# Performance work log

Hardware: AMD Instinct MI355X
Metric: run time of the kernel (lower is better)

Reference implementation:

```python
import jax, jax.numpy as jnp
import numpy as np

B = 256   # batch == nodes (required by the module's mask broadcasting)
N = 256
F = 128   # in_features
H = 4     # num_heads
D = 8     # out_features (per-head dim)
E_RAND = 8192


def setup_inputs() -> dict:
    key = jax.random.key(0)
    ks = jax.random.split(key, 10)
    x = jax.random.normal(ks[0], (B, N, F), jnp.float32)
    # random edges + self-loops so every adjacency row is non-empty
    e = jax.random.randint(ks[1], (2, E_RAND), 0, B)
    diag = jnp.stack([jnp.arange(B), jnp.arange(B)])
    edge_index = jnp.concatenate([e, diag], axis=1)  # [2, 8448]
    s_in = 1.0 / np.sqrt(F)
    s_hd = 1.0 / np.sqrt(H * D)
    Wq = jax.random.normal(ks[2], (F, H * D), jnp.float32) * s_in
    Wk = jax.random.normal(ks[3], (F, H * D), jnp.float32) * s_in
    Wv = jax.random.normal(ks[4], (F, H * D), jnp.float32) * s_in
    Wo = jax.random.normal(ks[5], (H * D, D), jnp.float32) * s_hd
    bq = jax.random.normal(ks[6], (H * D,), jnp.float32) * s_in
    bk = jax.random.normal(ks[7], (H * D,), jnp.float32) * s_in
    bv = jax.random.normal(ks[8], (H * D,), jnp.float32) * s_in
    bo = jax.random.normal(ks[9], (D,), jnp.float32) * s_hd
    return dict(x=x, edge_index=edge_index, Wq=Wq, bq=bq, Wk=Wk, bk=bk,
                Wv=Wv, bv=bv, Wo=Wo, bo=bo)


def reference(x, edge_index, Wq, bq, Wk, bk, Wv, bv, Wo, bo):
    Bn, Nn, _ = x.shape
    q = (x @ Wq + bq).reshape(Bn, Nn, H, D)
    k = (x @ Wk + bk).reshape(Bn, Nn, H, D)
    v = (x @ Wv + bv).reshape(Bn, Nn, H, D)
    # [B, H, N, N]
    scores = jnp.einsum('bqhd,bkhd->bhqk', q, k) / jnp.sqrt(jnp.float32(D))
    # dense adjacency from sparse edge list, as in the original
    adj = jnp.zeros((Bn, Bn), x.dtype).at[edge_index[0], edge_index[1]].set(1.0)
    # mask [B,B] broadcasts over trailing (q,k) dims since N == B
    scores = jnp.where(adj == 0, -jnp.inf, scores)
    attn = jax.nn.softmax(scores, axis=-1)
    out = jnp.einsum('bhqk,bkhd->bqhd', attn, v).reshape(Bn, Nn, H * D)
    return out @ Wo + bo
```

## Files before the change

### kernel.cpp

```cpp
#include <hip/hip_runtime.h>

typedef unsigned int u32;
typedef __fp16 h2v __attribute__((ext_vector_type(2)));
typedef __fp16 h4 __attribute__((ext_vector_type(4)));
typedef float f32x16 __attribute__((ext_vector_type(16)));

#define NB 256
#define NNODE 256
#define FF 128
#define DD 8
#define HDIM 32

__device__ __forceinline__ float dot2(h2v a, h2v b, float c) {
  return __builtin_amdgcn_fdot2(a, b, c, false);
}
__device__ __forceinline__ h2v bch2(u32 u) { return __builtin_bit_cast(h2v, u); }
__device__ __forceinline__ h4 bch4(uint2 u) { return __builtin_bit_cast(h4, u); }
__device__ __forceinline__ u32 bcu(h2v v) { return __builtin_bit_cast(u32, v); }
__device__ __forceinline__ f32x16 fzero() {
  f32x16 z;
  #pragma unroll
  for (int r = 0; r < 16; ++r) z[r] = 0.f;
  return z;
}
__device__ __forceinline__ f32x16 mfma8(h4 a, h4 b, f32x16 c) {
  return __builtin_amdgcn_mfma_f32_32x32x8f16(a, b, c, 0, 0, 0);
}

__global__ __launch_bounds__(256) void prep_kernel(
    const float* __restrict__ Wq, const float* __restrict__ bq,
    const float* __restrict__ Wk, const float* __restrict__ bk,
    const float* __restrict__ Wv, const float* __restrict__ bv,
    const float* __restrict__ Wo, const int* __restrict__ eidx, int E,
    u32* __restrict__ mask, u32* __restrict__ WtH, float* __restrict__ bias,
    u32* __restrict__ woT2)
{
  int g = blockIdx.x * 256 + threadIdx.x;
  if (g < 96 * 64) {
    int c = g >> 6, f = (g & 63) * 2;
    const float* W = (c < 32) ? Wq : ((c < 64) ? Wk : Wv);
    int cc = c & 31;
    WtH[g] = bcu(__builtin_amdgcn_cvt_pkrtz(W[f*HDIM + cc], W[(f+1)*HDIM + cc]));
  }
  if (g < 96) {
    const float* bb = (g < 32) ? bq : ((g < 64) ? bk : bv);
    bias[g] = bb[g & 31];
  }
  if (g < 128) {
    int d = g >> 4, p = g & 15;
    woT2[g] = bcu(__builtin_amdgcn_cvt_pkrtz(Wo[(2*p)*DD + d], Wo[(2*p+1)*DD + d]));
  }
  if (g < E) {
    int r = eidx[g], c = eidx[E + g];
    atomicOr(&mask[r*8 + (c >> 5)], 1u << (c & 31));
  }
}

__global__ __launch_bounds__(256, 2) void fused_kernel(
    const float* __restrict__ x, const u32* __restrict__ WtH,
    const float* __restrict__ bias, const u32* __restrict__ mask,
    const u32* __restrict__ woT2, const float* __restrict__ bo,
    float* __restrict__ out)
{
  __shared__ u32 wLds[96 * 66];
  __shared__ __fp16 kS[NNODE * 36];
  __shared__ __fp16 vt32[32 * 260];
  __shared__ __fp16 oS[128 * 36];
  __shared__ u32 woS[128];
  __shared__ float boS[8];

  int t = threadIdx.x, lane = t & 63, w = t >> 6;
  int l31 = lane & 31, hi = lane >> 5;
  int b = blockIdx.x & 255, half = blockIdx.x >> 8;

  for (int g = t; g < 96 * 64; g += 256)
    wLds[(g >> 6) * 66 + (g & 63)] = WtH[g];
  if (t < 128) woS[t] = woT2[t];
  if (t < 8) boS[t] = bo[t];

  f32x16 aq, ak0, av0, ak1, av1;
  #pragma unroll
  for (int r = 0; r < 16; ++r) aq[r] = bias[(r & 3) + 8*(r >> 2) + 4*hi];
  {
    float bk_ = bias[32 + l31], bv_ = bias[64 + l31];
    #pragma unroll
    for (int r = 0; r < 16; ++r) { ak0[r]=bk_; av0[r]=bv_; ak1[r]=bk_; av1[r]=bv_; }
  }

  int node = half*128 + w*32 + l31;
  uint4 m0 = *(const uint4*)(mask + node * 8);
  uint4 m1 = *(const uint4*)(mask + node * 8 + 4);
  u32 mw8[8] = { m0.x, m0.y, m0.z, m0.w, m1.x, m1.y, m1.z, m1.w };
  #pragma unroll
  for (int i = 0; i < 8; ++i) mw8[i] = hi ? (mw8[i] >> 4) : mw8[i];

  __syncthreads();

  const float* xr0 = x + ((size_t)b * NNODE + w*32 + l31) * FF + 4 * hi;
  const float* xr1 = xr0 + (size_t)128 * FF;
  float4 xc0 = *(const float4*)(xr0);
  float4 xc1 = *(const float4*)(xr1);
  #pragma unroll
  for (int ks = 0; ks < 16; ++ks) {
    float4 xn0, xn1;
    if (ks < 15) {
      xn0 = *(const float4*)(xr0 + (ks + 1) * 8);
      xn1 = *(const float4*)(xr1 + (ks + 1) * 8);
    }
    h2v a0 = __builtin_amdgcn_cvt_pkrtz(xc0.x, xc0.y);
    h2v b0 = __builtin_amdgcn_cvt_pkrtz(xc0.z, xc0.w);
    h4 f0 = __builtin_shufflevector(a0, b0, 0, 1, 2, 3);
    h2v a1 = __builtin_amdgcn_cvt_pkrtz(xc1.x, xc1.y);
    h2v b1 = __builtin_amdgcn_cvt_pkrtz(xc1.z, xc1.w);
    h4 f1 = __builtin_shufflevector(a1, b1, 0, 1, 2, 3);
    h4 wk = bch4(*(const uint2*)&wLds[(32 + l31)*66 + ks*4 + 2*hi]);
    h4 wv = bch4(*(const uint2*)&wLds[(64 + l31)*66 + ks*4 + 2*hi]);
    h4 wq = bch4(*(const uint2*)&wLds[l31*66 + ks*4 + 2*hi]);
    ak0 = mfma8(f0, wk, ak0);
    ak1 = mfma8(f1, wk, ak1);
    av0 = mfma8(f0, wv, av0);
    av1 = mfma8(f1, wv, av1);
    aq  = mfma8(wq, half ? f1 : f0, aq);
    xc0 = xn0; xc1 = xn1;
  }
  #pragma unroll
  for (int r = 0; r < 16; ++r) {
    int rc = (r & 3) + 8*(r >> 2) + 4*hi;
    int n0 = w*32 + rc, n1 = n0 + 128;
    kS[n0 * 36 + l31] = (__fp16)ak0[r];
    kS[n1 * 36 + l31] = (__fp16)ak1[r];
    vt32[l31 * 260 + n0] = (__fp16)av0[r];
    vt32[l31 * 260 + n1] = (__fp16)av1[r];
  }
  h4 Qf[4];
  #pragma unroll
  for (int h = 0; h < 4; ++h) {
    h2v qa = __builtin_amdgcn_cvt_pkrtz(aq[4*h],     aq[4*h + 1]);
    h2v qb = __builtin_amdgcn_cvt_pkrtz(aq[4*h + 2], aq[4*h + 3]);
    Qf[h] = __builtin_shufflevector(qa, qb, 0, 1, 2, 3);
  }
  __syncthreads();

  const float sc2 = 0.51006977f;
  const h2v one2 = bch2(0x3C003C00u);
  f32x16 accO[4] = { fzero(), fzero(), fzero(), fzero() };
  float lp[4] = { 0.f, 0.f, 0.f, 0.f };
  #pragma unroll
  for (int kt = 0; kt < 8; ++kt) {
    u32 mwh = mw8[kt];
    float mbv[16];
    #pragma unroll
    for (int r = 0; r < 16; ++r) {
      int bp = (r & 3) + 8*(r >> 2);
      mbv[r] = ((mwh >> bp) & 1u) ? -8.0f : -1e30f;
    }
    u32 pw[4][8];
    #pragma unroll
    for (int h = 0; h < 4; ++h) {
      h4 Kf = bch4(*(const uint2*)&kS[(kt*32 + l31)*36 + 8*h + 4*hi]);
      f32x16 T = mfma8(Kf, Qf[h], fzero());
      #pragma unroll
      for (int j = 0; j < 8; ++j) {
        float p0 = __builtin_amdgcn_exp2f(__builtin_fmaf(T[2*j],   sc2, mbv[2*j]));
        float p1 = __builtin_amdgcn_exp2f(__builtin_fmaf(T[2*j+1], sc2, mbv[2*j+1]));
        pw[h][j] = bcu(__builtin_amdgcn_cvt_pkrtz(p0, p1));
        lp[h] = dot2(bch2(pw[h][j]), one2, lp[h]);
      }
    }
    __builtin_amdgcn_s_setprio(1);
    #pragma unroll
    for (int kk = 0; kk < 4; ++kk) {
      h4 va = bch4(*(const uint2*)&vt32[l31*260 + kt*32 + kk*8 + 4*hi]);
      #pragma unroll
      for (int h = 0; h < 4; ++h)
        accO[h] = mfma8(va, bch4(make_uint2(pw[h][2*kk], pw[h][2*kk+1])), accO[h]);
    }
    __builtin_amdgcn_s_setprio(0);
  }
  #pragma unroll
  for (int h = 0; h < 4; ++h) {
    float lq = lp[h] + __shfl_xor(lp[h], 32);
    float inv = 1.0f / lq;
    h2v o0 = __builtin_amdgcn_cvt_pkrtz(accO[h][4*h]*inv,   accO[h][4*h+1]*inv);
    h2v o1 = __builtin_amdgcn_cvt_pkrtz(accO[h][4*h+2]*inv, accO[h][4*h+3]*inv);
    *(uint2*)&oS[(w*32 + l31)*36 + 8*h + 4*hi] = make_uint2(bcu(o0), bcu(o1));
  }
  __syncthreads();

  int pr = t >> 1, d4 = (t & 1) * 4;
  float r4[4] = { boS[d4], boS[d4+1], boS[d4+2], boS[d4+3] };
  #pragma unroll
  for (int p = 0; p < 16; ++p) {
    h2v o2 = bch2(*(const u32*)&oS[pr*36 + 2*p]);
    #pragma unroll
    for (int d = 0; d < 4; ++d)
      r4[d] = dot2(o2, bch2(woS[(d4 + d)*16 + p]), r4[d]);
  }
  float4 o = { r4[0], r4[1], r4[2], r4[3] };
  *(float4*)(out + ((size_t)b * NNODE + half*128 + pr) * DD + d4) = o;
}

extern "C" void kernel_launch(void* const* d_in, const int* in_sizes, int n_in,
                              void* d_out, int out_size, void* d_ws, size_t ws_size,
                              hipStream_t stream)
{
  const float* x  = (const float*)d_in[0];
  const int*   ei = (const int*)d_in[1];
  const float* Wq = (const float*)d_in[2];
  const float* bq = (const float*)d_in[3];
  const float* Wk = (const float*)d_in[4];
  const float* bk = (const float*)d_in[5];
  const float* Wv = (const float*)d_in[6];
  const float* bv = (const float*)d_in[7];
  const float* Wo = (const float*)d_in[8];
  const float* bo = (const float*)d_in[9];
  int E = in_sizes[1] / 2;

  char* ws = (char*)d_ws;
  u32*   mask = (u32*)(ws + 0);
  u32*   WtH  = (u32*)(ws + 8192);
  float* bias = (float*)(ws + 32768);
  u32*   woT2 = (u32*)(ws + 33280);

  hipMemsetAsync(mask, 0, NNODE * 8 * sizeof(u32), stream);
  int prep_work = (96*64 > E) ? 96*64 : E;
  prep_kernel<<<(prep_work + 255)/256, 256, 0, stream>>>(
      Wq, bq, Wk, bk, Wv, bv, Wo, ei, E, mask, WtH, bias, woT2);
  fused_kernel<<<NB * 2, 256, 0, stream>>>(x, WtH, bias, mask, woT2, bo,
                                           (float*)d_out);
}
```

Before: 39.50 us.

## Switch to 32x32x16 f16 MFMA with permlane32 swaps for P operand

Replaces the 32x32x8 f16 MFMA with the gfx950 32x32x16 variant in both the QKV projection and the PV product, halving the instruction count. The P fragments produced by the score MFMA are rearranged across lane halves with v_permlane32_swap so they match the wider K operand layout. LDS pads change to fit 16-byte reads, and the output staging buffer now reuses the weight LDS region to cut shared memory. This risks layout mistakes in the swap mapping and adds permute instructions to the inner loop.

```diff
diff --git a/kernel.cpp b/kernel.cpp
--- a/kernel.cpp
+++ b/kernel.cpp
@@ -3,6 +3,7 @@
 typedef unsigned int u32;
 typedef __fp16 h2v __attribute__((ext_vector_type(2)));
 typedef __fp16 h4 __attribute__((ext_vector_type(4)));
+typedef __fp16 h8 __attribute__((ext_vector_type(8)));
 typedef float f32x16 __attribute__((ext_vector_type(16)));
 
 #define NB 256
@@ -16,6 +17,7 @@
 }
 __device__ __forceinline__ h2v bch2(u32 u) { return __builtin_bit_cast(h2v, u); }
 __device__ __forceinline__ h4 bch4(uint2 u) { return __builtin_bit_cast(h4, u); }
+__device__ __forceinline__ h8 bch8(uint4 u) { return __builtin_bit_cast(h8, u); }
 __device__ __forceinline__ u32 bcu(h2v v) { return __builtin_bit_cast(u32, v); }
 __device__ __forceinline__ f32x16 fzero() {
   f32x16 z;
@@ -25,6 +27,9 @@
 }
 __device__ __forceinline__ f32x16 mfma8(h4 a, h4 b, f32x16 c) {
   return __builtin_amdgcn_mfma_f32_32x32x8f16(a, b, c, 0, 0, 0);
+}
+__device__ __forceinline__ f32x16 mfma16(h8 a, h8 b, f32x16 c) {
+  return __builtin_amdgcn_mfma_f32_32x32x16_f16(a, b, c, 0, 0, 0);
 }
 
 __global__ __launch_bounds__(256) void prep_kernel(
@@ -62,19 +67,19 @@
     const u32* __restrict__ woT2, const float* __restrict__ bo,
     float* __restrict__ out)
 {
-  __shared__ u32 wLds[96 * 66];
+  __shared__ u32 wLds[96 * 68];
   __shared__ __fp16 kS[NNODE * 36];
-  __shared__ __fp16 vt32[32 * 260];
-  __shared__ __fp16 oS[128 * 36];
+  __shared__ __fp16 vt32[32 * 264];
   __shared__ u32 woS[128];
   __shared__ float boS[8];
+  __fp16* oS = (__fp16*)wLds;
 
   int t = threadIdx.x, lane = t & 63, w = t >> 6;
   int l31 = lane & 31, hi = lane >> 5;
   int b = blockIdx.x & 255, half = blockIdx.x >> 8;
 
   for (int g = t; g < 96 * 64; g += 256)
-    wLds[(g >> 6) * 66 + (g & 63)] = WtH[g];
+    wLds[(g >> 6) * 68 + (g & 63)] = WtH[g];
   if (t < 128) woS[t] = woT2[t];
   if (t < 8) boS[t] = bo[t];
 
@@ -96,32 +101,36 @@
 
   __syncthreads();
 
-  const float* xr0 = x + ((size_t)b * NNODE + w*32 + l31) * FF + 4 * hi;
+  const float* xr0 = x + ((size_t)b * NNODE + w*32 + l31) * FF + 8 * hi;
   const float* xr1 = xr0 + (size_t)128 * FF;
-  float4 xc0 = *(const float4*)(xr0);
-  float4 xc1 = *(const float4*)(xr1);
-  #pragma unroll
-  for (int ks = 0; ks < 16; ++ks) {
-    float4 xn0, xn1;
-    if (ks < 15) {
-      xn0 = *(const float4*)(xr0 + (ks + 1) * 8);
-      xn1 = *(const float4*)(xr1 + (ks + 1) * 8);
-    }
-    h2v a0 = __builtin_amdgcn_cvt_pkrtz(xc0.x, xc0.y);
-    h2v b0 = __builtin_amdgcn_cvt_pkrtz(xc0.z, xc0.w);
-    h4 f0 = __builtin_shufflevector(a0, b0, 0, 1, 2, 3);
-    h2v a1 = __builtin_amdgcn_cvt_pkrtz(xc1.x, xc1.y);
-    h2v b1 = __builtin_amdgcn_cvt_pkrtz(xc1.z, xc1.w);
-    h4 f1 = __builtin_shufflevector(a1, b1, 0, 1, 2, 3);
-    h4 wk = bch4(*(const uint2*)&wLds[(32 + l31)*66 + ks*4 + 2*hi]);
-    h4 wv = bch4(*(const uint2*)&wLds[(64 + l31)*66 + ks*4 + 2*hi]);
-    h4 wq = bch4(*(const uint2*)&wLds[l31*66 + ks*4 + 2*hi]);
-    ak0 = mfma8(f0, wk, ak0);
-    ak1 = mfma8(f1, wk, ak1);
-    av0 = mfma8(f0, wv, av0);
-    av1 = mfma8(f1, wv, av1);
-    aq  = mfma8(wq, half ? f1 : f0, aq);
-    xc0 = xn0; xc1 = xn1;
+  float4 xc0a = *(const float4*)(xr0),     xc0b = *(const float4*)(xr0 + 4);
+  float4 xc1a = *(const float4*)(xr1),     xc1b = *(const float4*)(xr1 + 4);
+  #pragma unroll
+  for (int ks = 0; ks < 8; ++ks) {
+    float4 xn0a, xn0b, xn1a, xn1b;
+    if (ks < 7) {
+      xn0a = *(const float4*)(xr0 + (ks + 1) * 16);
+      xn0b = *(const float4*)(xr0 + (ks + 1) * 16 + 4);
+      xn1a = *(const float4*)(xr1 + (ks + 1) * 16);
+      xn1b = *(const float4*)(xr1 + (ks + 1) * 16 + 4);
+    }
+    h8 f0 = bch8(make_uint4(bcu(__builtin_amdgcn_cvt_pkrtz(xc0a.x, xc0a.y)),
+                            bcu(__builtin_amdgcn_cvt_pkrtz(xc0a.z, xc0a.w)),
+                            bcu(__builtin_amdgcn_cvt_pkrtz(xc0b.x, xc0b.y)),
+                            bcu(__builtin_amdgcn_cvt_pkrtz(xc0b.z, xc0b.w))));
+    h8 f1 = bch8(make_uint4(bcu(__builtin_amdgcn_cvt_pkrtz(xc1a.x, xc1a.y)),
+                            bcu(__builtin_amdgcn_cvt_pkrtz(xc1a.z, xc1a.w)),
+                            bcu(__builtin_amdgcn_cvt_pkrtz(xc1b.x, xc1b.y)),
+                            bcu(__builtin_amdgcn_cvt_pkrtz(xc1b.z, xc1b.w))));
+    h8 wk = bch8(*(const uint4*)&wLds[(32 + l31)*68 + ks*8 + 4*hi]);
+    h8 wv = bch8(*(const uint4*)&wLds[(64 + l31)*68 + ks*8 + 4*hi]);
+    h8 wq = bch8(*(const uint4*)&wLds[l31*68 + ks*8 + 4*hi]);
+    ak0 = mfma16(f0, wk, ak0);
+    ak1 = mfma16(f1, wk, ak1);
+    av0 = mfma16(f0, wv, av0);
+    av1 = mfma16(f1, wv, av1);
+    aq  = mfma16(wq, half ? f1 : f0, aq);
+    xc0a = xn0a; xc0b = xn0b; xc1a = xn1a; xc1b = xn1b;
   }
   #pragma unroll
   for (int r = 0; r < 16; ++r) {
@@ -129,8 +138,8 @@
     int n0 = w*32 + rc, n1 = n0 + 128;
     kS[n0 * 36 + l31] = (__fp16)ak0[r];
     kS[n1 * 36 + l31] = (__fp16)ak1[r];
-    vt32[l31 * 260 + n0] = (__fp16)av0[r];
-    vt32[l31 * 260 + n1] = (__fp16)av1[r];
+    vt32[l31 * 264 + n0] = (__fp16)av0[r];
+    vt32[l31 * 264 + n1] = (__fp16)av1[r];
   }
   h4 Qf[4];
   #pragma unroll
@@ -167,13 +176,19 @@
         lp[h] = dot2(bch2(pw[h][j]), one2, lp[h]);
       }
     }
+    h8 va0 = bch8(*(const uint4*)&vt32[l31*264 + kt*32 + 8*hi]);
+    h8 va1 = bch8(*(const uint4*)&vt32[l31*264 + kt*32 + 16 + 8*hi]);
     __builtin_amdgcn_s_setprio(1);
     #pragma unroll
-    for (int kk = 0; kk < 4; ++kk) {
-      h4 va = bch4(*(const uint2*)&vt32[l31*260 + kt*32 + kk*8 + 4*hi]);
-      #pragma unroll
-      for (int h = 0; h < 4; ++h)
-        accO[h] = mfma8(va, bch4(make_uint2(pw[h][2*kk], pw[h][2*kk+1])), accO[h]);
+    for (int h = 0; h < 4; ++h) {
+      u32 a0 = pw[h][0], a1 = pw[h][1], a2 = pw[h][2], a3 = pw[h][3];
+      asm("v_permlane32_swap_b32 %0, %1" : "+v"(a0), "+v"(a2));
+      asm("v_permlane32_swap_b32 %0, %1" : "+v"(a1), "+v"(a3));
+      accO[h] = mfma16(va0, bch8(make_uint4(a0, a1, a2, a3)), accO[h]);
+      u32 c0 = pw[h][4], c1 = pw[h][5], c2 = pw[h][6], c3 = pw[h][7];
+      asm("v_permlane32_swap_b32 %0, %1" : "+v"(c0), "+v"(c2));
+      asm("v_permlane32_swap_b32 %0, %1" : "+v"(c1), "+v"(c3));
+      accO[h] = mfma16(va1, bch8(make_uint4(c0, c1, c2, c3)), accO[h]);
     }
     __builtin_amdgcn_s_setprio(0);
   }
```

Measured after the change: 38.28 us. 3.1% less time.
